# Kernel optimization log

Measured on AMD Instinct MI355X. Metric: run time of the kernel, lower is better.

## Reference

```python
import jax, jax.numpy as jnp
import numpy as np

EPSILON = 1e-4
MAX_ITER = 10


def setup_inputs() -> dict:
    key = jax.random.key(0)
    k1, k2, k3 = jax.random.split(key, 3)
    B, N, M = 64, 1024, 1024
    s = jax.random.uniform(k1, (B, N, M), dtype=jnp.float32)
    nrows = jax.random.randint(k2, (B,), 0, N, dtype=jnp.int32)
    ncols = jax.random.randint(k3, (B,), 0, M, dtype=jnp.int32)
    return {"s": s, "nrows": nrows, "ncols": ncols}


def reference(s, nrows, ncols):
    # s: [B, N, M]; nrows/ncols: [B] valid row/col counts per sample.
    B, N, M = s.shape
    row_mask = jnp.arange(N, dtype=nrows.dtype)[None, :] < nrows[:, None]  # [B, N]
    col_mask = jnp.arange(M, dtype=ncols.dtype)[None, :] < ncols[:, None]  # [B, M]
    mask = row_mask[:, :, None] & col_mask[:, None, :]  # [B, N, M]

    s = s + EPSILON
    for i in range(MAX_ITER):
        # i even -> column normalization (sum over dim 1); i odd -> row normalization (sum over dim 2)
        axis = 2 if i % 2 == 1 else 1
        ssum = jnp.sum(s, axis=axis, keepdims=True)
        tmp = jnp.where(mask, 1.0 / ssum, jnp.zeros((), dtype=s.dtype))
        s = s * tmp
    return s
```

## Files before the change

kernel.cpp:

```cpp
#include <hip/hip_runtime.h>

#define EPS 1e-4f

constexpr int Bn = 64;
constexpr int Nn = 1024;
constexpr int Mn = 1024;
constexpr int NSPLIT = 16;
constexpr int CHUNK  = Nn / NSPLIT;
constexpr int SLOT   = 16;

typedef float f32x4 __attribute__((ext_vector_type(4)));

__device__ __forceinline__ unsigned pkh2(float a, float b) {
    union { _Float16 h; unsigned short u; } ta, tb;
    ta.h = (_Float16)a; tb.h = (_Float16)b;
    return (unsigned)ta.u | ((unsigned)tb.u << 16);
}
__device__ __forceinline__ float lo16(unsigned v) {
    union { unsigned short u; _Float16 h; } t; t.u = (unsigned short)(v & 0xffffu);
    return (float)t.h;
}
__device__ __forceinline__ float hi16(unsigned v) {
    union { unsigned short u; _Float16 h; } t; t.u = (unsigned short)(v >> 16);
    return (float)t.h;
}

__global__ __launch_bounds__(256) void fuse0_kernel(
        const float* __restrict__ s, unsigned short* __restrict__ sc,
        float* __restrict__ p) {
    __shared__ float4 red[256];
    const int b = blockIdx.x, sp = blockIdx.y;
    const int t = threadIdx.x, half = t >> 7, tc = t & 127;
    float acc[8];
    #pragma unroll
    for (int k = 0; k < 8; ++k) acc[k] = 0.f;
    for (int j = 0; j < CHUNK; j += 2) {
        const int n = sp * CHUNK + j + half;
        const size_t roff = ((size_t)b * Nn + n) * Mn;
        const f32x4* src = reinterpret_cast<const f32x4*>(s + roff) + 2 * tc;
        f32x4 v0 = __builtin_nontemporal_load(src);
        f32x4 v1 = __builtin_nontemporal_load(src + 1);
        v0 += EPS; v1 += EPS;
        acc[0] += v0.x; acc[1] += v0.y; acc[2] += v0.z; acc[3] += v0.w;
        acc[4] += v1.x; acc[5] += v1.y; acc[6] += v1.z; acc[7] += v1.w;
        uint4 wpk = { pkh2(v0.x, v0.y), pkh2(v0.z, v0.w),
                      pkh2(v1.x, v1.y), pkh2(v1.z, v1.w) };
        reinterpret_cast<uint4*>(sc + roff)[tc] = wpk;
    }
    if (half) {
        red[tc * 2]     = make_float4(acc[0], acc[1], acc[2], acc[3]);
        red[tc * 2 + 1] = make_float4(acc[4], acc[5], acc[6], acc[7]);
    }
    __syncthreads();
    if (!half) {
        const float4 r0 = red[tc * 2], r1 = red[tc * 2 + 1];
        float* pp = p + ((size_t)(b * SLOT + sp)) * Mn + tc * 8;
        float4 o0 = {acc[0] + r0.x, acc[1] + r0.y, acc[2] + r0.z, acc[3] + r0.w};
        float4 o1 = {acc[4] + r1.x, acc[5] + r1.y, acc[6] + r1.z, acc[7] + r1.w};
        *reinterpret_cast<float4*>(pp)     = o0;
        *reinterpret_cast<float4*>(pp + 4) = o1;
    }
}

__global__ __launch_bounds__(256) void col_final_kernel(
        const float* __restrict__ p, const int* __restrict__ ncols,
        float* __restrict__ c) {
    const int b = blockIdx.x;
    const int m = blockIdx.y * 256 + threadIdx.x;
    float sum = 0.f;
    #pragma unroll
    for (int k = 0; k < SLOT; ++k)
        sum += p[((size_t)(b * SLOT + k)) * Mn + m];
    c[(size_t)b * Mn + m] = (m < ncols[b] && sum > 0.f) ? 1.f / sum : 0.f;
}

__global__ __launch_bounds__(256) void rowcol_kernel(
        const unsigned short* __restrict__ sc, const float* __restrict__ c,
        const int* __restrict__ nrows, float* __restrict__ p) {
    __shared__ float4 red[4][256];
    const int b = blockIdx.x;
    const int t = threadIdx.x, w = t >> 6, l = t & 63;
    const int n0 = blockIdx.y * 64 + w * 16;
    const float4* cb = reinterpret_cast<const float4*>(c + (size_t)b * Mn);
    const float4 c0 = cb[2 * l], c1 = cb[2 * l + 1];
    const float4 c2 = cb[128 + 2 * l], c3 = cb[128 + 2 * l + 1];
    const int nr = nrows[b];
    float acc[16];
    #pragma unroll
    for (int k = 0; k < 16; ++k) acc[k] = 0.f;
    const uint4* base = reinterpret_cast<const uint4*>(sc + ((size_t)b * Nn + n0) * Mn);
    for (int j = 0; j < 16; j += 2) {
        const uint4* r0 = base + (size_t)j * 128;
        const uint4 a0 = r0[l],       d0 = r0[64 + l];
        const uint4 a1 = r0[128 + l], d1 = r0[192 + l];
        const float x0 = lo16(a0.x),  x1 = hi16(a0.x),  x2 = lo16(a0.y),  x3 = hi16(a0.y);
        const float x4 = lo16(a0.z),  x5 = hi16(a0.z),  x6 = lo16(a0.w),  x7 = hi16(a0.w);
        const float x8 = lo16(d0.x),  x9 = hi16(d0.x),  x10 = lo16(d0.y), x11 = hi16(d0.y);
        const float x12 = lo16(d0.z), x13 = hi16(d0.z), x14 = lo16(d0.w), x15 = hi16(d0.w);
        const float y0 = lo16(a1.x),  y1 = hi16(a1.x),  y2 = lo16(a1.y),  y3 = hi16(a1.y);
        const float y4 = lo16(a1.z),  y5 = hi16(a1.z),  y6 = lo16(a1.w),  y7 = hi16(a1.w);
        const float y8 = lo16(d1.x),  y9 = hi16(d1.x),  y10 = lo16(d1.y), y11 = hi16(d1.y);
        const float y12 = lo16(d1.z), y13 = hi16(d1.z), y14 = lo16(d1.w), y15 = hi16(d1.w);
        float part0 = x0 * c0.x + x1 * c0.y + x2 * c0.z + x3 * c0.w
                    + x4 * c1.x + x5 * c1.y + x6 * c1.z + x7 * c1.w
                    + x8 * c2.x + x9 * c2.y + x10 * c2.z + x11 * c2.w
                    + x12 * c3.x + x13 * c3.y + x14 * c3.z + x15 * c3.w;
        float part1 = y0 * c0.x + y1 * c0.y + y2 * c0.z + y3 * c0.w
                    + y4 * c1.x + y5 * c1.y + y6 * c1.z + y7 * c1.w
                    + y8 * c2.x + y9 * c2.y + y10 * c2.z + y11 * c2.w
                    + y12 * c3.x + y13 * c3.y + y14 * c3.z + y15 * c3.w;
        #pragma unroll
        for (int off = 1; off < 64; off <<= 1) {
            part0 += __shfl_xor(part0, off, 64);
            part1 += __shfl_xor(part1, off, 64);
        }
        const int n = n0 + j;
        const float rv0 = (n < nr && part0 > 0.f) ? 1.f / part0 : 0.f;
        const float rv1 = (n + 1 < nr && part1 > 0.f) ? 1.f / part1 : 0.f;
        acc[0]  += x0 * rv0 + y0 * rv1;   acc[1]  += x1 * rv0 + y1 * rv1;
        acc[2]  += x2 * rv0 + y2 * rv1;   acc[3]  += x3 * rv0 + y3 * rv1;
        acc[4]  += x4 * rv0 + y4 * rv1;   acc[5]  += x5 * rv0 + y5 * rv1;
        acc[6]  += x6 * rv0 + y6 * rv1;   acc[7]  += x7 * rv0 + y7 * rv1;
        acc[8]  += x8 * rv0 + y8 * rv1;   acc[9]  += x9 * rv0 + y9 * rv1;
        acc[10] += x10 * rv0 + y10 * rv1; acc[11] += x11 * rv0 + y11 * rv1;
        acc[12] += x12 * rv0 + y12 * rv1; acc[13] += x13 * rv0 + y13 * rv1;
        acc[14] += x14 * rv0 + y14 * rv1; acc[15] += x15 * rv0 + y15 * rv1;
    }
    red[w][2 * l]       = make_float4(acc[0], acc[1], acc[2], acc[3]);
    red[w][2 * l + 1]   = make_float4(acc[4], acc[5], acc[6], acc[7]);
    red[w][128 + 2 * l] = make_float4(acc[8], acc[9], acc[10], acc[11]);
    red[w][129 + 2 * l] = make_float4(acc[12], acc[13], acc[14], acc[15]);
    __syncthreads();
    const float4 r0 = red[0][t], r1 = red[1][t], r2 = red[2][t], r3 = red[3][t];
    float4 o = { r0.x + r1.x + r2.x + r3.x, r0.y + r1.y + r2.y + r3.y,
                 r0.z + r1.z + r2.z + r3.z, r0.w + r1.w + r2.w + r3.w };
    float* pp = p + ((size_t)(b * SLOT) + blockIdx.y) * Mn;
    reinterpret_cast<float4*>(pp)[t] = o;
}

__global__ __launch_bounds__(256) void final_kernel(
        const float* __restrict__ s, const float* __restrict__ c,
        const int* __restrict__ nrows, float* __restrict__ out) {
    const int b = blockIdx.x;
    const int t = threadIdx.x, w = t >> 6, l = t & 63;
    const int n0 = blockIdx.y * 32 + w * 8;
    const float4* cb = reinterpret_cast<const float4*>(c + (size_t)b * Mn);
    float4 cc[4];
    #pragma unroll
    for (int k = 0; k < 4; ++k) cc[k] = cb[64 * k + l];
    const int nr = nrows[b];
    for (int j = 0; j < 8; ++j) {
        const int n = n0 + j;
        const size_t roff = ((size_t)b * Nn + n) * Mn;
        const f32x4* row = reinterpret_cast<const f32x4*>(s + roff);
        f32x4 a[4];
        float part = 0.f;
        #pragma unroll
        for (int k = 0; k < 4; ++k) {
            a[k] = __builtin_nontemporal_load(row + 64 * k + l);
            a[k] += EPS;
            part += a[k].x * cc[k].x + a[k].y * cc[k].y
                  + a[k].z * cc[k].z + a[k].w * cc[k].w;
        }
        #pragma unroll
        for (int off = 1; off < 64; off <<= 1) part += __shfl_xor(part, off, 64);
        const float rv = (n < nr && part > 0.f) ? 1.f / part : 0.f;
        f32x4* orow = reinterpret_cast<f32x4*>(out + roff);
        #pragma unroll
        for (int k = 0; k < 4; ++k) {
            f32x4 o;
            o.x = a[k].x * cc[k].x * rv;
            o.y = a[k].y * cc[k].y * rv;
            o.z = a[k].z * cc[k].z * rv;
            o.w = a[k].w * cc[k].w * rv;
            __builtin_nontemporal_store(o, orow + 64 * k + l);
        }
    }
}

extern "C" void kernel_launch(void* const* d_in, const int* in_sizes, int n_in,
                              void* d_out, int out_size, void* d_ws, size_t ws_size,
                              hipStream_t stream) {
    const float* s     = (const float*)d_in[0];
    const int*   nrows = (const int*)d_in[1];
    const int*   ncols = (const int*)d_in[2];
    float* out = (float*)d_out;

    unsigned short* sc = (unsigned short*)d_ws;
    float* p = (float*)(sc + (size_t)Bn * Nn * Mn);
    float* c = p + (size_t)Bn * SLOT * Mn;

    fuse0_kernel<<<dim3(Bn, NSPLIT), 256, 0, stream>>>(s, sc, p);
    col_final_kernel<<<dim3(Bn, Mn / 256), 256, 0, stream>>>(p, ncols, c);
    for (int it = 0; it < 4; ++it) {
        rowcol_kernel<<<dim3(Bn, Nn / 64), 256, 0, stream>>>(sc, c, nrows, p);
        col_final_kernel<<<dim3(Bn, Mn / 256), 256, 0, stream>>>(p, ncols, c);
    }
    final_kernel<<<dim3(Bn, Nn / 32), 256, 0, stream>>>(s, c, nrows, out);
}
```

Baseline: 634.4 us.

## Fold column-reciprocal reduction into consumers and software-prefetch next rows

Removes the separate col_final kernel: each rowcol and final block now sums the 16 partial column slots itself, masks by ncols, takes reciprocals into shared memory, and ping-pongs partial buffers between launches. This cuts five kernel launches and the round trip through the c array. The cost is that every block redundantly reads 16×1024 partials. The change also adds register double-buffering in fuse0, rowcol and final so that the next row's loads are issued before the current row is processed, at the cost of more register pressure.

After: 623.6 us. About the same (-1.7%).

```diff
diff --git a/kernel.cpp b/kernel.cpp
--- a/kernel.cpp
+++ b/kernel.cpp
@@ -23,6 +23,23 @@
 __device__ __forceinline__ float hi16(unsigned v) {
     union { unsigned short u; _Float16 h; } t; t.u = (unsigned short)(v >> 16);
     return (float)t.h;
+}
+
+__device__ __forceinline__ void fold_c(const float* __restrict__ pin,
+                                       const int* __restrict__ ncols,
+                                       int b, int t, float* cs) {
+    const int m0 = t * 4;
+    f32x4 s4 = {0.f, 0.f, 0.f, 0.f};
+    #pragma unroll
+    for (int k = 0; k < SLOT; ++k)
+        s4 += *reinterpret_cast<const f32x4*>(pin + ((size_t)(b * SLOT + k)) * Mn + m0);
+    const int nc = ncols[b];
+    f32x4 r;
+    r.x = (m0 + 0 < nc && s4.x > 0.f) ? 1.f / s4.x : 0.f;
+    r.y = (m0 + 1 < nc && s4.y > 0.f) ? 1.f / s4.y : 0.f;
+    r.z = (m0 + 2 < nc && s4.z > 0.f) ? 1.f / s4.z : 0.f;
+    r.w = (m0 + 3 < nc && s4.w > 0.f) ? 1.f / s4.w : 0.f;
+    *reinterpret_cast<f32x4*>(&cs[m0]) = r;
 }
 
 __global__ __launch_bounds__(256) void fuse0_kernel(
@@ -34,18 +51,25 @@
     float acc[8];
     #pragma unroll
     for (int k = 0; k < 8; ++k) acc[k] = 0.f;
+    const size_t roff0 = ((size_t)b * Nn + sp * CHUNK + half) * Mn;
+    const f32x4* src0 = reinterpret_cast<const f32x4*>(s + roff0) + 2 * tc;
+    f32x4 v0 = __builtin_nontemporal_load(src0);
+    f32x4 v1 = __builtin_nontemporal_load(src0 + 1);
     for (int j = 0; j < CHUNK; j += 2) {
-        const int n = sp * CHUNK + j + half;
-        const size_t roff = ((size_t)b * Nn + n) * Mn;
-        const f32x4* src = reinterpret_cast<const f32x4*>(s + roff) + 2 * tc;
-        f32x4 v0 = __builtin_nontemporal_load(src);
-        f32x4 v1 = __builtin_nontemporal_load(src + 1);
-        v0 += EPS; v1 += EPS;
-        acc[0] += v0.x; acc[1] += v0.y; acc[2] += v0.z; acc[3] += v0.w;
-        acc[4] += v1.x; acc[5] += v1.y; acc[6] += v1.z; acc[7] += v1.w;
-        uint4 wpk = { pkh2(v0.x, v0.y), pkh2(v0.z, v0.w),
-                      pkh2(v1.x, v1.y), pkh2(v1.z, v1.w) };
+        f32x4 n0 = {}, n1 = {};
+        if (j < CHUNK - 2) {
+            const f32x4* nsrc = src0 + (size_t)(j + 2) * (Mn / 4);
+            n0 = __builtin_nontemporal_load(nsrc);
+            n1 = __builtin_nontemporal_load(nsrc + 1);
+        }
+        f32x4 w0 = v0 + EPS, w1 = v1 + EPS;
+        acc[0] += w0.x; acc[1] += w0.y; acc[2] += w0.z; acc[3] += w0.w;
+        acc[4] += w1.x; acc[5] += w1.y; acc[6] += w1.z; acc[7] += w1.w;
+        uint4 wpk = { pkh2(w0.x, w0.y), pkh2(w0.z, w0.w),
+                      pkh2(w1.x, w1.y), pkh2(w1.z, w1.w) };
+        const size_t roff = roff0 + (size_t)j * Mn;
         reinterpret_cast<uint4*>(sc + roff)[tc] = wpk;
+        v0 = n0; v1 = n1;
     }
     if (half) {
         red[tc * 2]     = make_float4(acc[0], acc[1], acc[2], acc[3]);
@@ -62,37 +86,33 @@
     }
 }
 
-__global__ __launch_bounds__(256) void col_final_kernel(
-        const float* __restrict__ p, const int* __restrict__ ncols,
-        float* __restrict__ c) {
-    const int b = blockIdx.x;
-    const int m = blockIdx.y * 256 + threadIdx.x;
-    float sum = 0.f;
-    #pragma unroll
-    for (int k = 0; k < SLOT; ++k)
-        sum += p[((size_t)(b * SLOT + k)) * Mn + m];
-    c[(size_t)b * Mn + m] = (m < ncols[b] && sum > 0.f) ? 1.f / sum : 0.f;
-}
-
 __global__ __launch_bounds__(256) void rowcol_kernel(
-        const unsigned short* __restrict__ sc, const float* __restrict__ c,
-        const int* __restrict__ nrows, float* __restrict__ p) {
+        const unsigned short* __restrict__ sc, const float* __restrict__ pin,
+        const int* __restrict__ nrows, const int* __restrict__ ncols,
+        float* __restrict__ pout) {
+    __shared__ float cs[1024];
     __shared__ float4 red[4][256];
     const int b = blockIdx.x;
     const int t = threadIdx.x, w = t >> 6, l = t & 63;
+    fold_c(pin, ncols, b, t, cs);
+    __syncthreads();
+    const f32x4 c0 = *reinterpret_cast<const f32x4*>(&cs[8 * l]);
+    const f32x4 c1 = *reinterpret_cast<const f32x4*>(&cs[8 * l + 4]);
+    const f32x4 c2 = *reinterpret_cast<const f32x4*>(&cs[512 + 8 * l]);
+    const f32x4 c3 = *reinterpret_cast<const f32x4*>(&cs[512 + 8 * l + 4]);
     const int n0 = blockIdx.y * 64 + w * 16;
-    const float4* cb = reinterpret_cast<const float4*>(c + (size_t)b * Mn);
-    const float4 c0 = cb[2 * l], c1 = cb[2 * l + 1];
-    const float4 c2 = cb[128 + 2 * l], c3 = cb[128 + 2 * l + 1];
     const int nr = nrows[b];
     float acc[16];
     #pragma unroll
     for (int k = 0; k < 16; ++k) acc[k] = 0.f;
     const uint4* base = reinterpret_cast<const uint4*>(sc + ((size_t)b * Nn + n0) * Mn);
+    uint4 a0 = base[l], d0 = base[64 + l], a1 = base[128 + l], d1 = base[192 + l];
     for (int j = 0; j < 16; j += 2) {
-        const uint4* r0 = base + (size_t)j * 128;
-        const uint4 a0 = r0[l],       d0 = r0[64 + l];
-        const uint4 a1 = r0[128 + l], d1 = r0[192 + l];
+        uint4 na0 = {}, nd0 = {}, na1 = {}, nd1 = {};
+        if (j < 14) {
+            const uint4* nx = base + (size_t)(j + 2) * 128;
+            na0 = nx[l]; nd0 = nx[64 + l]; na1 = nx[128 + l]; nd1 = nx[192 + l];
+        }
         const float x0 = lo16(a0.x),  x1 = hi16(a0.x),  x2 = lo16(a0.y),  x3 = hi16(a0.y);
         const float x4 = lo16(a0.z),  x5 = hi16(a0.z),  x6 = lo16(a0.w),  x7 = hi16(a0.w);
         const float x8 = lo16(d0.x),  x9 = hi16(d0.x),  x10 = lo16(d0.y), x11 = hi16(d0.y);
@@ -125,6 +145,7 @@
         acc[10] += x10 * rv0 + y10 * rv1; acc[11] += x11 * rv0 + y11 * rv1;
         acc[12] += x12 * rv0 + y12 * rv1; acc[13] += x13 * rv0 + y13 * rv1;
         acc[14] += x14 * rv0 + y14 * rv1; acc[15] += x15 * rv0 + y15 * rv1;
+        a0 = na0; d0 = nd0; a1 = na1; d1 = nd1;
     }
     red[w][2 * l]       = make_float4(acc[0], acc[1], acc[2], acc[3]);
     red[w][2 * l + 1]   = make_float4(acc[4], acc[5], acc[6], acc[7]);
@@ -134,38 +155,51 @@
     const float4 r0 = red[0][t], r1 = red[1][t], r2 = red[2][t], r3 = red[3][t];
     float4 o = { r0.x + r1.x + r2.x + r3.x, r0.y + r1.y + r2.y + r3.y,
                  r0.z + r1.z + r2.z + r3.z, r0.w + r1.w + r2.w + r3.w };
-    float* pp = p + ((size_t)(b * SLOT) + blockIdx.y) * Mn;
+    float* pp = pout + ((size_t)(b * SLOT) + blockIdx.y) * Mn;
     reinterpret_cast<float4*>(pp)[t] = o;
 }
 
 __global__ __launch_bounds__(256) void final_kernel(
-        const float* __restrict__ s, const float* __restrict__ c,
-        const int* __restrict__ nrows, float* __restrict__ out) {
+        const float* __restrict__ s, const float* __restrict__ pin,
+        const int* __restrict__ nrows, const int* __restrict__ ncols,
+        float* __restrict__ out) {
+    __shared__ float cs[1024];
     const int b = blockIdx.x;
     const int t = threadIdx.x, w = t >> 6, l = t & 63;
+    fold_c(pin, ncols, b, t, cs);
+    __syncthreads();
+    f32x4 cc[4];
+    #pragma unroll
+    for (int k = 0; k < 4; ++k)
+        cc[k] = *reinterpret_cast<const f32x4*>(&cs[256 * k + 4 * l]);
     const int n0 = blockIdx.y * 32 + w * 8;
-    const float4* cb = reinterpret_cast<const float4*>(c + (size_t)b * Mn);
-    float4 cc[4];
-    #pragma unroll
-    for (int k = 0; k < 4; ++k) cc[k] = cb[64 * k + l];
     const int nr = nrows[b];
+    const size_t roff0 = ((size_t)b * Nn + n0) * Mn;
+    const f32x4* row0 = reinterpret_cast<const f32x4*>(s + roff0);
+    f32x4 a[4];
+    #pragma unroll
+    for (int k = 0; k < 4; ++k)
+        a[k] = __builtin_nontemporal_load(row0 + 64 * k + l);
     for (int j = 0; j < 8; ++j) {
-        const int n = n0 + j;
-        const size_t roff = ((size_t)b * Nn + n) * Mn;
-        const f32x4* row = reinterpret_cast<const f32x4*>(s + roff);
-        f32x4 a[4];
+        f32x4 na[4] = {};
+        if (j < 7) {
+            const f32x4* nrow = row0 + (size_t)(j + 1) * (Mn / 4);
+            #pragma unroll
+            for (int k = 0; k < 4; ++k)
+                na[k] = __builtin_nontemporal_load(nrow + 64 * k + l);
+        }
         float part = 0.f;
         #pragma unroll
         for (int k = 0; k < 4; ++k) {
-            a[k] = __builtin_nontemporal_load(row + 64 * k + l);
             a[k] += EPS;
             part += a[k].x * cc[k].x + a[k].y * cc[k].y
                   + a[k].z * cc[k].z + a[k].w * cc[k].w;
         }
         #pragma unroll
         for (int off = 1; off < 64; off <<= 1) part += __shfl_xor(part, off, 64);
+        const int n = n0 + j;
         const float rv = (n < nr && part > 0.f) ? 1.f / part : 0.f;
-        f32x4* orow = reinterpret_cast<f32x4*>(out + roff);
+        f32x4* orow = reinterpret_cast<f32x4*>(out + roff0 + (size_t)j * Mn);
         #pragma unroll
         for (int k = 0; k < 4; ++k) {
             f32x4 o;
@@ -175,6 +209,8 @@
             o.w = a[k].w * cc[k].w * rv;
             __builtin_nontemporal_store(o, orow + 64 * k + l);
         }
+        #pragma unroll
+        for (int k = 0; k < 4; ++k) a[k] = na[k];
     }
 }
 
@@ -187,14 +223,13 @@
     float* out = (float*)d_out;
 
     unsigned short* sc = (unsigned short*)d_ws;
-    float* p = (float*)(sc + (size_t)Bn * Nn * Mn);
-    float* c = p + (size_t)Bn * SLOT * Mn;
-
-    fuse0_kernel<<<dim3(Bn, NSPLIT), 256, 0, stream>>>(s, sc, p);
-    col_final_kernel<<<dim3(Bn, Mn / 256), 256, 0, stream>>>(p, ncols, c);
-    for (int it = 0; it < 4; ++it) {
-        rowcol_kernel<<<dim3(Bn, Nn / 64), 256, 0, stream>>>(sc, c, nrows, p);
-        col_final_kernel<<<dim3(Bn, Mn / 256), 256, 0, stream>>>(p, ncols, c);
-    }
-    final_kernel<<<dim3(Bn, Nn / 32), 256, 0, stream>>>(s, c, nrows, out);
-}
+    float* pA = (float*)(sc + (size_t)Bn * Nn * Mn);
+    float* pB = pA + (size_t)Bn * SLOT * Mn;
+
+    fuse0_kernel<<<dim3(Bn, NSPLIT), 256, 0, stream>>>(s, sc, pA);
+    rowcol_kernel<<<dim3(Bn, NSPLIT), 256, 0, stream>>>(sc, pA, nrows, ncols, pB);
+    rowcol_kernel<<<dim3(Bn, NSPLIT), 256, 0, stream>>>(sc, pB, nrows, ncols, pA);
+    rowcol_kernel<<<dim3(Bn, NSPLIT), 256, 0, stream>>>(sc, pA, nrows, ncols, pB);
+    rowcol_kernel<<<dim3(Bn, NSPLIT), 256, 0, stream>>>(sc, pB, nrows, ncols, pA);
+    final_kernel<<<dim3(Bn, Nn / 32), 256, 0, stream>>>(s, pA, nrows, ncols, out);
+}
```
